# Optimization experiments

Measured on AMD Instinct MI355X. Metric: run time of the kernel, lower is better.

The kernel has to match this reference:

```python
import jax, jax.numpy as jnp
import numpy as np

B, L, E = 2, 2048, 1024
NH, DH = 16, 64          # num_heads, attn_hidden_size
HID = 4096               # FFN hidden_size
EPS = 1e-5


def _layernorm(x, g, b):
    mu = jnp.mean(x, axis=-1, keepdims=True)
    var = jnp.var(x, axis=-1, keepdims=True)
    return (x - mu) * jax.lax.rsqrt(var + EPS) * g + b


def setup_inputs() -> dict:
    key = jax.random.key(0)
    ks = jax.random.split(key, 12)
    s = 0.02
    return {
        "x":    jax.random.normal(ks[0], (B, L, E), dtype=jnp.float32),
        "Wa":   jax.random.normal(ks[1], (E, NH * 3 * DH), dtype=jnp.float32) * s,
        "Wout": jax.random.normal(ks[2], (NH * DH, E), dtype=jnp.float32) * s,
        "bout": jnp.zeros((E,), dtype=jnp.float32),
        "W1":   jax.random.normal(ks[3], (E, HID), dtype=jnp.float32) * s,
        "b1":   jnp.zeros((HID,), dtype=jnp.float32),
        "W2":   jax.random.normal(ks[4], (HID, E), dtype=jnp.float32) * s,
        "b2":   jnp.zeros((E,), dtype=jnp.float32),
        "g1":   jnp.ones((E,), dtype=jnp.float32),
        "be1":  jnp.zeros((E,), dtype=jnp.float32),
        "g2":   jnp.ones((E,), dtype=jnp.float32),
        "be2":  jnp.zeros((E,), dtype=jnp.float32),
    }


def _attention(o, Wa, Wout, bout):
    b, l, e = o.shape
    tmp = o @ Wa                                   # (b, l, nh*3*dh)
    tmp = tmp.reshape(b, l, NH, 3 * DH).transpose(0, 2, 1, 3)  # (b, nh, l, 3dh)
    q, k, v = jnp.split(tmp, 3, axis=-1)           # each (b, nh, l, dh)
    scores = jnp.einsum('bhqd,bhkd->bhqk', q, k) / np.sqrt(DH)
    causal = jnp.tril(jnp.ones((l, l), dtype=bool))
    scores = jnp.where(causal, scores, -jnp.inf)
    A = jax.nn.softmax(scores, axis=-1)
    out = jnp.einsum('bhqk,bhkd->bhqd', A, v)      # (b, nh, l, dh)
    out = out.transpose(0, 2, 1, 3).reshape(b, l, NH * DH)
    return out @ Wout + bout


def reference(x, Wa, Wout, bout, W1, b1, W2, b2, g1, be1, g2, be2):
    o = _layernorm(x, g1, be1)
    o = _attention(o, Wa, Wout, bout)
    o = _layernorm(x + o, g2, be2)
    o = o @ W1 + b1          # activation is Identity
    o = x + (o @ W2 + b2)
    return o
```

## Files before the change

### kernel.cpp

```cpp
#include <hip/hip_runtime.h>
#include <hip/hip_bf16.h>

#define BB 2
#define LL 2048
#define EE 1024
#define NHH 16
#define DHH 64
#define HIDD 4096
#define MTOK (BB*LL)
#define NQKV (NHH*3*DHH)

typedef __attribute__((ext_vector_type(8))) short bf16x8;
typedef __attribute__((ext_vector_type(4))) float f32x4;

#define MFMA16(a,b,c) __builtin_amdgcn_mfma_f32_16x16x32_bf16(a,b,c,0,0,0)

static __device__ __forceinline__ void gload_lds16(const void* g, void* lds) {
  __builtin_amdgcn_global_load_lds(
      (const __attribute__((address_space(1))) unsigned int*)g,
      (__attribute__((address_space(3))) unsigned int*)lds, 16, 0, 0);
}

__global__ __launch_bounds__(256)
void convT_kernel(const float* __restrict__ W, __hip_bfloat16* __restrict__ WT,
                  int K, int N) {
  __shared__ float tile[32][33];
  const int tx = threadIdx.x & 31, ty = threadIdx.x >> 5;
  const int n0 = blockIdx.x * 32, k0 = blockIdx.y * 32;
#pragma unroll
  for (int i = 0; i < 4; ++i)
    tile[ty + i*8][tx] = W[(size_t)(k0 + ty + i*8) * N + n0 + tx];
  __syncthreads();
#pragma unroll
  for (int i = 0; i < 4; ++i)
    WT[(size_t)(n0 + ty + i*8) * K + k0 + tx] = __float2bfloat16(tile[tx][ty + i*8]);
}

__global__ __launch_bounds__(256)
void vtrans_kernel(const __hip_bfloat16* __restrict__ qkv,
                   __hip_bfloat16* __restrict__ VT) {
  __shared__ ushort tile[32][34];
  const int tx = threadIdx.x & 31, ty = threadIdx.x >> 5;
  const int tok0 = blockIdx.x * 32;
  const int dh0  = blockIdx.y * 32;
  const int bh   = blockIdx.z;
  const int b = bh >> 4, h = bh & 15;
  const ushort* src = (const ushort*)qkv;
#pragma unroll
  for (int i = 0; i < 4; ++i)
    tile[ty + i*8][tx] =
      src[(size_t)(b*LL + tok0 + ty + i*8) * NQKV + h*192 + 128 + dh0 + tx];
  __syncthreads();
  ushort* dst = (ushort*)VT;
#pragma unroll
  for (int i = 0; i < 4; ++i)
    dst[(size_t)(bh*DHH + dh0 + ty + i*8) * LL + tok0 + tx] = tile[tx][ty + i*8];
}

__global__ __launch_bounds__(256)
void ln_kernel(const float* __restrict__ in, const float* __restrict__ g,
               const float* __restrict__ be, __hip_bfloat16* __restrict__ out) {
  const int row = blockIdx.x;
  const int t = threadIdx.x;
  const float4 v = ((const float4*)(in + (size_t)row * EE))[t];
  float s = v.x + v.y + v.z + v.w;
  float q = v.x*v.x + v.y*v.y + v.z*v.z + v.w*v.w;
#pragma unroll
  for (int off = 32; off >= 1; off >>= 1) {
    s += __shfl_xor(s, off);
    q += __shfl_xor(q, off);
  }
  __shared__ float ps[4], pq[4];
  if ((t & 63) == 0) { ps[t >> 6] = s; pq[t >> 6] = q; }
  __syncthreads();
  s = ps[0] + ps[1] + ps[2] + ps[3];
  q = pq[0] + pq[1] + pq[2] + pq[3];
  const float mean = s * (1.0f / EE);
  const float rstd = rsqrtf(q * (1.0f / EE) - mean * mean + 1e-5f);
  const float4 gg = ((const float4*)g)[t];
  const float4 bb = ((const float4*)be)[t];
  union { ushort4 u; __hip_bfloat16 h[4]; } o;
  o.h[0] = __float2bfloat16((v.x - mean) * rstd * gg.x + bb.x);
  o.h[1] = __float2bfloat16((v.y - mean) * rstd * gg.y + bb.y);
  o.h[2] = __float2bfloat16((v.z - mean) * rstd * gg.z + bb.z);
  o.h[3] = __float2bfloat16((v.w - mean) * rstd * gg.w + bb.w);
  ((ushort4*)(out + (size_t)row * EE))[t] = o.u;
}

template<int OUT_BF16, int HAS_BIAS, int HAS_RES>
__global__ __launch_bounds__(256)
void gemm_kernel(const __hip_bfloat16* __restrict__ A,
                 const __hip_bfloat16* __restrict__ BT,
                 void* __restrict__ Cv,
                 const float* __restrict__ bias,
                 const float* __restrict__ res,
                 int M, int N, int K) {
  __shared__ alignas(16) __hip_bfloat16 sA[128 * 32];
  __shared__ alignas(16) __hip_bfloat16 sB[128 * 32];
  const int t = threadIdx.x;
  const int wv = t >> 6;
  const int l = t & 63;
  const int lr = l & 15;
  const int lk = (l >> 4) * 8;
  const int m0 = blockIdx.y * 128;
  const int n0 = blockIdx.x * 128;
  const int wrow = (wv >> 1) * 64;
  const int wcol = (wv & 1) * 64;

  const int srow = t >> 2;
  const int scol = (t & 3) * 8;
  const __hip_bfloat16* gA = A + (size_t)(m0 + srow) * K + scol;
  const __hip_bfloat16* gB = BT + (size_t)(n0 + srow) * K + scol;
  char* ldsA = (char*)sA + wv * 1024;
  char* ldsB = (char*)sB + wv * 1024;

  f32x4 acc[4][4] = {};

  for (int k0 = 0; k0 < K; k0 += 32) {
    gload_lds16(gA + k0, ldsA);
    gload_lds16(gA + (size_t)64 * K + k0, ldsA + 4096);
    gload_lds16(gB + k0, ldsB);
    gload_lds16(gB + (size_t)64 * K + k0, ldsB + 4096);
    __syncthreads();
    bf16x8 af[4], bfv[4];
#pragma unroll
    for (int mi = 0; mi < 4; ++mi)
      af[mi] = *(const bf16x8*)(sA + (wrow + mi * 16 + lr) * 32 + lk);
#pragma unroll
    for (int ni = 0; ni < 4; ++ni)
      bfv[ni] = *(const bf16x8*)(sB + (wcol + ni * 16 + lr) * 32 + lk);
#pragma unroll
    for (int mi = 0; mi < 4; ++mi)
#pragma unroll
      for (int ni = 0; ni < 4; ++ni)
        acc[mi][ni] = MFMA16(af[mi], bfv[ni], acc[mi][ni]);
    __syncthreads();
  }

  const int rbase = (l >> 4) * 4;
#pragma unroll
  for (int mi = 0; mi < 4; ++mi) {
#pragma unroll
    for (int ni = 0; ni < 4; ++ni) {
#pragma unroll
      for (int r = 0; r < 4; ++r) {
        const int row = m0 + wrow + mi * 16 + rbase + r;
        const int col = n0 + wcol + ni * 16 + lr;
        float v = acc[mi][ni][r];
        if constexpr (HAS_BIAS) v += bias[col];
        if constexpr (HAS_RES)  v += res[(size_t)row * N + col];
        if constexpr (OUT_BF16)
          ((__hip_bfloat16*)Cv)[(size_t)row * N + col] = __float2bfloat16(v);
        else
          ((float*)Cv)[(size_t)row * N + col] = v;
      }
    }
  }
}

__global__ __launch_bounds__(256)
void attn_kernel(const __hip_bfloat16* __restrict__ qkv,
                 const __hip_bfloat16* __restrict__ VT,
                 __hip_bfloat16* __restrict__ out) {
  __shared__ alignas(16) __hip_bfloat16 sP[4][32 * 72];
  const int t = threadIdx.x;
  const int wv = t >> 6, l = t & 63;
  const int lr = l & 15, lg = l >> 4, lk = lg * 8;
  const int hh = blockIdx.y, b = blockIdx.z;
  int qx = blockIdx.x;
  if (b == 1) qx = 15 - qx;
  const int qw = qx * 128 + wv * 32;
  const size_t rowbase = (size_t)b * LL;
  const int hoff = hh * (3 * DHH);
  const __hip_bfloat16* vt = VT + (size_t)((b * NHH + hh) * DHH) * LL;

  bf16x8 qa[2][2];
#pragma unroll
  for (int rg = 0; rg < 2; ++rg)
#pragma unroll
    for (int h = 0; h < 2; ++h)
      qa[rg][h] = *(const bf16x8*)(qkv + (rowbase + qw + rg*16 + lr) * NQKV
                                   + hoff + h*32 + lk);

  f32x4 o[2][4] = {};
  float mrun[2][4], lrun[2][4];
#pragma unroll
  for (int rg = 0; rg < 2; ++rg)
#pragma unroll
    for (int r = 0; r < 4; ++r) { mrun[rg][r] = -INFINITY; lrun[rg][r] = 0.f; }

  __hip_bfloat16* sp = sP[wv];
  const int nt = (qw + 95) >> 6;

  for (int kt = 0; kt < nt; ++kt) {
    const int t0 = kt * 64;
    bf16x8 vb[4][2];
#pragma unroll
    for (int ni = 0; ni < 4; ++ni)
#pragma unroll
      for (int ks = 0; ks < 2; ++ks)
        vb[ni][ks] = *(const bf16x8*)(vt + (size_t)(ni*16 + lr) * LL + t0 + ks*32 + lk);

    f32x4 s[2][4];
#pragma unroll
    for (int tg = 0; tg < 4; ++tg) {
      const __hip_bfloat16* kp = qkv + (rowbase + t0 + tg*16 + lr) * NQKV + hoff + DHH;
      bf16x8 kb0 = *(const bf16x8*)(kp + lk);
      bf16x8 kb1 = *(const bf16x8*)(kp + 32 + lk);
#pragma unroll
      for (int rg = 0; rg < 2; ++rg) {
        f32x4 z = {0.f, 0.f, 0.f, 0.f};
        z = MFMA16(qa[rg][0], kb0, z);
        z = MFMA16(qa[rg][1], kb1, z);
        s[rg][tg] = z;
      }
    }

    const bool edge = (kt == nt - 1);
#pragma unroll
    for (int rg = 0; rg < 2; ++rg)
#pragma unroll
      for (int tg = 0; tg < 4; ++tg)
#pragma unroll
        for (int r = 0; r < 4; ++r) {
          float v = s[rg][tg][r] * 0.125f;
          if (edge) {
            const int tok = t0 + tg*16 + lr;
            const int qr  = qw + rg*16 + lg*4 + r;
            if (tok > qr) v = -INFINITY;
          }
          s[rg][tg][r] = v;
        }

#pragma unroll
    for (int rg = 0; rg < 2; ++rg)
#pragma unroll
      for (int r = 0; r < 4; ++r) {
        float m = fmaxf(fmaxf(s[rg][0][r], s[rg][1][r]),
                        fmaxf(s[rg][2][r], s[rg][3][r]));
#pragma unroll
        for (int off = 8; off >= 1; off >>= 1)
          m = fmaxf(m, __shfl_xor(m, off));
        const float mnew = fmaxf(mrun[rg][r], m);
        const float corr = __expf(mrun[rg][r] - mnew);
        const float p0 = __expf(s[rg][0][r] - mnew);
        const float p1 = __expf(s[rg][1][r] - mnew);
        const float p2 = __expf(s[rg][2][r] - mnew);
        const float p3 = __expf(s[rg][3][r] - mnew);
        float rs = (p0 + p1) + (p2 + p3);
#pragma unroll
        for (int off = 8; off >= 1; off >>= 1)
          rs += __shfl_xor(rs, off);
        lrun[rg][r] = lrun[rg][r] * corr + rs;
        mrun[rg][r] = mnew;
        const int q = rg*16 + lg*4 + r;
        sp[q*72 +      lr] = __float2bfloat16(p0);
        sp[q*72 + 16 + lr] = __float2bfloat16(p1);
        sp[q*72 + 32 + lr] = __float2bfloat16(p2);
        sp[q*72 + 48 + lr] = __float2bfloat16(p3);
#pragma unroll
        for (int ni = 0; ni < 4; ++ni) o[rg][ni][r] *= corr;
      }

#pragma unroll
    for (int rg = 0; rg < 2; ++rg) {
      bf16x8 pf0 = *(const bf16x8*)(sp + (rg*16 + lr)*72 + lk);
      bf16x8 pf1 = *(const bf16x8*)(sp + (rg*16 + lr)*72 + 32 + lk);
#pragma unroll
      for (int ni = 0; ni < 4; ++ni) {
        o[rg][ni] = MFMA16(pf0, vb[ni][0], o[rg][ni]);
        o[rg][ni] = MFMA16(pf1, vb[ni][1], o[rg][ni]);
      }
    }
  }

#pragma unroll
  for (int rg = 0; rg < 2; ++rg)
#pragma unroll
    for (int r = 0; r < 4; ++r) {
      const float inv = 1.0f / lrun[rg][r];
      const int qr = qw + rg*16 + lg*4 + r;
      __hip_bfloat16* op = out + (rowbase + qr) * (NHH * DHH) + hh * DHH;
#pragma unroll
      for (int ni = 0; ni < 4; ++ni)
        op[ni*16 + lr] = __float2bfloat16(o[rg][ni][r] * inv);
    }
}

extern "C" void kernel_launch(void* const* d_in, const int* in_sizes, int n_in,
                              void* d_out, int out_size, void* d_ws, size_t ws_size,
                              hipStream_t stream) {
  (void)in_sizes; (void)n_in; (void)out_size; (void)ws_size;
  const float* x    = (const float*)d_in[0];
  const float* Wa   = (const float*)d_in[1];
  const float* Wout = (const float*)d_in[2];
  const float* bout = (const float*)d_in[3];
  const float* W1   = (const float*)d_in[4];
  const float* b1   = (const float*)d_in[5];
  const float* W2   = (const float*)d_in[6];
  const float* b2   = (const float*)d_in[7];
  const float* g1   = (const float*)d_in[8];
  const float* be1  = (const float*)d_in[9];
  const float* g2   = (const float*)d_in[10];
  const float* be2  = (const float*)d_in[11];

  char* ws = (char*)d_ws;
  __hip_bfloat16* WaT   = (__hip_bfloat16*)(ws + 0);
  __hip_bfloat16* WoutT = (__hip_bfloat16*)(ws + 6291456);
  __hip_bfloat16* W1T   = (__hip_bfloat16*)(ws + 8388608);
  __hip_bfloat16* W2T   = (__hip_bfloat16*)(ws + 16777216);
  __hip_bfloat16* o1    = (__hip_bfloat16*)(ws + 25165824);
  __hip_bfloat16* qkv   = (__hip_bfloat16*)(ws + 33554432);
  __hip_bfloat16* hbuf  = (__hip_bfloat16*)(ws + 25165824);
  __hip_bfloat16* attnb = (__hip_bfloat16*)(ws + 58720256);
  __hip_bfloat16* ln2b  = (__hip_bfloat16*)(ws + 58720256);
  float*          ybuf  = (float*)(ws + 67108864);
  __hip_bfloat16* VT    = (__hip_bfloat16*)(ws + 67108864);

  convT_kernel<<<dim3(NQKV/32, EE/32), 256, 0, stream>>>(Wa, WaT, EE, NQKV);
  convT_kernel<<<dim3(EE/32, EE/32), 256, 0, stream>>>(Wout, WoutT, EE, EE);
  convT_kernel<<<dim3(HIDD/32, EE/32), 256, 0, stream>>>(W1, W1T, EE, HIDD);
  convT_kernel<<<dim3(EE/32, HIDD/32), 256, 0, stream>>>(W2, W2T, HIDD, EE);
  ln_kernel<<<MTOK, 256, 0, stream>>>(x, g1, be1, o1);
  gemm_kernel<1,0,0><<<dim3(NQKV/128, MTOK/128), 256, 0, stream>>>(
      o1, WaT, qkv, nullptr, nullptr, MTOK, NQKV, EE);
  vtrans_kernel<<<dim3(LL/32, DHH/32, BB*NHH), 256, 0, stream>>>(qkv, VT);
  attn_kernel<<<dim3(LL/128, NHH, BB), 256, 0, stream>>>(qkv, VT, attnb);
  gemm_kernel<0,1,1><<<dim3(EE/128, MTOK/128), 256, 0, stream>>>(
      attnb, WoutT, ybuf, bout, x, MTOK, EE, EE);
  ln_kernel<<<MTOK, 256, 0, stream>>>(ybuf, g2, be2, ln2b);
  gemm_kernel<1,1,0><<<dim3(HIDD/128, MTOK/128), 256, 0, stream>>>(
      ln2b, W1T, hbuf, b1, nullptr, MTOK, HIDD, EE);
  gemm_kernel<0,1,1><<<dim3(EE/128, MTOK/128), 256, 0, stream>>>(
      hbuf, W2T, (float*)d_out, b2, x, MTOK, EE, HIDD);
}
```

Baseline: 437.7 us.

## Double-buffer GEMM LDS tiles, swizzle workgroups, split-K the FFN2 GEMM

Rewrites the GEMM as a body with two LDS buffers so the next K-slice's global-to-LDS loads are issued while the current slice is computed. It also adds a workgroup index remap meant to improve L2 reuse. The FFN2 GEMM becomes a split-K launch with 128x64 tiles writing two fp32 partial buffers, followed by a reduction kernel that adds bias and residual; this targets the small-grid occupancy problem of the K=4096 GEMM at the cost of extra partial-buffer traffic. Workspace buffers are reassigned so the partials fit.

Result: faster. 402.4 us (-8.0%).

```diff
diff --git a/kernel.cpp b/kernel.cpp
--- a/kernel.cpp
+++ b/kernel.cpp
@@ -87,53 +87,65 @@
   ((ushort4*)(out + (size_t)row * EE))[t] = o.u;
 }
 
-template<int OUT_BF16, int HAS_BIAS, int HAS_RES>
-__global__ __launch_bounds__(256)
-void gemm_kernel(const __hip_bfloat16* __restrict__ A,
-                 const __hip_bfloat16* __restrict__ BT,
-                 void* __restrict__ Cv,
-                 const float* __restrict__ bias,
-                 const float* __restrict__ res,
-                 int M, int N, int K) {
-  __shared__ alignas(16) __hip_bfloat16 sA[128 * 32];
-  __shared__ alignas(16) __hip_bfloat16 sB[128 * 32];
+template<int BN, int OUT_BF16, int HAS_BIAS, int HAS_RES>
+__device__ __forceinline__ void gemm_body(
+    const __hip_bfloat16* __restrict__ A, const __hip_bfloat16* __restrict__ BT,
+    void* __restrict__ Cv, const float* __restrict__ bias,
+    const float* __restrict__ res, int M, int N, int K, int lda, int ldb) {
+  constexpr int NF = BN / 32;
+  __shared__ alignas(16) __hip_bfloat16 sA[2][128 * 32];
+  __shared__ alignas(16) __hip_bfloat16 sB[2][BN * 32];
   const int t = threadIdx.x;
-  const int wv = t >> 6;
-  const int l = t & 63;
-  const int lr = l & 15;
-  const int lk = (l >> 4) * 8;
-  const int m0 = blockIdx.y * 128;
-  const int n0 = blockIdx.x * 128;
+  const int wv = t >> 6, l = t & 63;
+  const int lr = l & 15, lk = (l >> 4) * 8;
+
+  const int nwg = gridDim.x * gridDim.y;
+  int wg = blockIdx.y * gridDim.x + blockIdx.x;
+  wg = (wg & 7) * (nwg >> 3) + (wg >> 3);
+  const int bx = wg % gridDim.x, by = wg / gridDim.x;
+  const int m0 = by * 128, n0 = bx * BN;
+
   const int wrow = (wv >> 1) * 64;
-  const int wcol = (wv & 1) * 64;
-
-  const int srow = t >> 2;
-  const int scol = (t & 3) * 8;
-  const __hip_bfloat16* gA = A + (size_t)(m0 + srow) * K + scol;
-  const __hip_bfloat16* gB = BT + (size_t)(n0 + srow) * K + scol;
-  char* ldsA = (char*)sA + wv * 1024;
-  char* ldsB = (char*)sB + wv * 1024;
-
-  f32x4 acc[4][4] = {};
-
-  for (int k0 = 0; k0 < K; k0 += 32) {
-    gload_lds16(gA + k0, ldsA);
-    gload_lds16(gA + (size_t)64 * K + k0, ldsA + 4096);
-    gload_lds16(gB + k0, ldsB);
-    gload_lds16(gB + (size_t)64 * K + k0, ldsB + 4096);
+  const int wcol = (wv & 1) * (BN / 2);
+  const int srow = t >> 2, scol = (t & 3) * 8;
+  const __hip_bfloat16* gA = A + (size_t)(m0 + srow) * lda + scol;
+  const __hip_bfloat16* gB = BT + (size_t)(n0 + srow) * ldb + scol;
+
+  auto stage = [&](int buf, int k0) {
+    char* dA = (char*)(&sA[buf][0]) + wv * 1024;
+    gload_lds16(gA + k0, dA);
+    gload_lds16(gA + (size_t)64 * lda + k0, dA + 4096);
+    char* dB = (char*)(&sB[buf][0]) + wv * 1024;
+    gload_lds16(gB + k0, dB);
+    if constexpr (BN == 128)
+      gload_lds16(gB + (size_t)64 * ldb + k0, dB + 4096);
+  };
+
+  f32x4 acc[4][NF] = {};
+
+  auto compute = [&](int buf) {
+    bf16x8 af[4], bfv[NF];
+#pragma unroll
+    for (int mi = 0; mi < 4; ++mi)
+      af[mi] = *(const bf16x8*)(&sA[buf][(wrow + mi * 16 + lr) * 32 + lk]);
+#pragma unroll
+    for (int ni = 0; ni < NF; ++ni)
+      bfv[ni] = *(const bf16x8*)(&sB[buf][(wcol + ni * 16 + lr) * 32 + lk]);
+#pragma unroll
+    for (int mi = 0; mi < 4; ++mi)
+#pragma unroll
+      for (int ni = 0; ni < NF; ++ni)
+        acc[mi][ni] = MFMA16(af[mi], bfv[ni], acc[mi][ni]);
+  };
+
+  stage(0, 0);
+  __syncthreads();
+  for (int k0 = 0; k0 < K; k0 += 64) {
+    stage(1, k0 + 32);
+    compute(0);
     __syncthreads();
-    bf16x8 af[4], bfv[4];
-#pragma unroll
-    for (int mi = 0; mi < 4; ++mi)
-      af[mi] = *(const bf16x8*)(sA + (wrow + mi * 16 + lr) * 32 + lk);
-#pragma unroll
-    for (int ni = 0; ni < 4; ++ni)
-      bfv[ni] = *(const bf16x8*)(sB + (wcol + ni * 16 + lr) * 32 + lk);
-#pragma unroll
-    for (int mi = 0; mi < 4; ++mi)
-#pragma unroll
-      for (int ni = 0; ni < 4; ++ni)
-        acc[mi][ni] = MFMA16(af[mi], bfv[ni], acc[mi][ni]);
+    if (k0 + 64 < K) stage(0, k0 + 64);
+    compute(1);
     __syncthreads();
   }
 
@@ -141,7 +153,7 @@
 #pragma unroll
   for (int mi = 0; mi < 4; ++mi) {
 #pragma unroll
-    for (int ni = 0; ni < 4; ++ni) {
+    for (int ni = 0; ni < NF; ++ni) {
 #pragma unroll
       for (int r = 0; r < 4; ++r) {
         const int row = m0 + wrow + mi * 16 + rbase + r;
@@ -155,6 +167,46 @@
           ((float*)Cv)[(size_t)row * N + col] = v;
       }
     }
+  }
+}
+
+__global__ __launch_bounds__(256)
+void gemm_qkv(const __hip_bfloat16* A, const __hip_bfloat16* BT, __hip_bfloat16* C) {
+  gemm_body<128,1,0,0>(A, BT, C, nullptr, nullptr, MTOK, NQKV, EE, EE, EE);
+}
+__global__ __launch_bounds__(256)
+void gemm_wout(const __hip_bfloat16* A, const __hip_bfloat16* BT, float* C,
+               const float* bias, const float* res) {
+  gemm_body<128,0,1,1>(A, BT, C, bias, res, MTOK, EE, EE, EE, EE);
+}
+__global__ __launch_bounds__(256)
+void gemm_ffn1(const __hip_bfloat16* A, const __hip_bfloat16* BT, __hip_bfloat16* C,
+               const float* bias) {
+  gemm_body<128,1,1,0>(A, BT, C, bias, nullptr, MTOK, HIDD, EE, EE, EE);
+}
+__global__ __launch_bounds__(256)
+void gemm_ffn2p(const __hip_bfloat16* A, const __hip_bfloat16* BT,
+                float* P0, float* P1) {
+  const int ks = blockIdx.z;
+  float* P = ks ? P1 : P0;
+  gemm_body<64,0,0,0>(A + ks * 2048, BT + ks * 2048, P, nullptr, nullptr,
+                      MTOK, EE, 2048, HIDD, HIDD);
+}
+
+__global__ __launch_bounds__(256)
+void ffn2_reduce(const float4* __restrict__ P0, const float4* __restrict__ P1,
+                 const float4* __restrict__ x, const float* __restrict__ b2,
+                 float4* __restrict__ out) {
+  const int n4 = MTOK * EE / 4;
+  for (int i = blockIdx.x * 256 + threadIdx.x; i < n4; i += 2048 * 256) {
+    const float4 b = ((const float4*)b2)[i & 255];
+    const float4 p = P0[i], q = P1[i], xx = x[i];
+    float4 o;
+    o.x = xx.x + b.x + p.x + q.x;
+    o.y = xx.y + b.y + p.y + q.y;
+    o.z = xx.z + b.z + p.z + q.z;
+    o.w = xx.w + b.w + p.w + q.w;
+    out[i] = o;
   }
 }
 
@@ -311,26 +363,26 @@
   __hip_bfloat16* W2T   = (__hip_bfloat16*)(ws + 16777216);
   __hip_bfloat16* o1    = (__hip_bfloat16*)(ws + 25165824);
   __hip_bfloat16* qkv   = (__hip_bfloat16*)(ws + 33554432);
-  __hip_bfloat16* hbuf  = (__hip_bfloat16*)(ws + 25165824);
-  __hip_bfloat16* attnb = (__hip_bfloat16*)(ws + 58720256);
-  __hip_bfloat16* ln2b  = (__hip_bfloat16*)(ws + 58720256);
-  float*          ybuf  = (float*)(ws + 67108864);
-  __hip_bfloat16* VT    = (__hip_bfloat16*)(ws + 67108864);
+  __hip_bfloat16* VT    = (__hip_bfloat16*)(ws + 58720256);
+  __hip_bfloat16* attnb = (__hip_bfloat16*)(ws + 67108864);
+  float*          ybuf  = (float*)(ws + 33554432);
+  __hip_bfloat16* ln2b  = (__hip_bfloat16*)(ws + 25165824);
+  __hip_bfloat16* hbuf  = (__hip_bfloat16*)(ws + 50331648);
+  float*          P0    = (float*)(ws + 0);
+  float*          P1    = (float*)(ws + 33554432);
 
   convT_kernel<<<dim3(NQKV/32, EE/32), 256, 0, stream>>>(Wa, WaT, EE, NQKV);
   convT_kernel<<<dim3(EE/32, EE/32), 256, 0, stream>>>(Wout, WoutT, EE, EE);
   convT_kernel<<<dim3(HIDD/32, EE/32), 256, 0, stream>>>(W1, W1T, EE, HIDD);
   convT_kernel<<<dim3(EE/32, HIDD/32), 256, 0, stream>>>(W2, W2T, HIDD, EE);
   ln_kernel<<<MTOK, 256, 0, stream>>>(x, g1, be1, o1);
-  gemm_kernel<1,0,0><<<dim3(NQKV/128, MTOK/128), 256, 0, stream>>>(
-      o1, WaT, qkv, nullptr, nullptr, MTOK, NQKV, EE);
+  gemm_qkv<<<dim3(NQKV/128, MTOK/128), 256, 0, stream>>>(o1, WaT, qkv);
   vtrans_kernel<<<dim3(LL/32, DHH/32, BB*NHH), 256, 0, stream>>>(qkv, VT);
   attn_kernel<<<dim3(LL/128, NHH, BB), 256, 0, stream>>>(qkv, VT, attnb);
-  gemm_kernel<0,1,1><<<dim3(EE/128, MTOK/128), 256, 0, stream>>>(
-      attnb, WoutT, ybuf, bout, x, MTOK, EE, EE);
+  gemm_wout<<<dim3(EE/128, MTOK/128), 256, 0, stream>>>(attnb, WoutT, ybuf, bout, x);
   ln_kernel<<<MTOK, 256, 0, stream>>>(ybuf, g2, be2, ln2b);
-  gemm_kernel<1,1,0><<<dim3(HIDD/128, MTOK/128), 256, 0, stream>>>(
-      ln2b, W1T, hbuf, b1, nullptr, MTOK, HIDD, EE);
-  gemm_kernel<0,1,1><<<dim3(EE/128, MTOK/128), 256, 0, stream>>>(
-      hbuf, W2T, (float*)d_out, b2, x, MTOK, EE, HIDD);
-}
+  gemm_ffn1<<<dim3(HIDD/128, MTOK/128), 256, 0, stream>>>(ln2b, W1T, hbuf, b1);
+  gemm_ffn2p<<<dim3(EE/64, MTOK/128, 2), 256, 0, stream>>>(hbuf, W2T, P0, P1);
+  ffn2_reduce<<<2048, 256, 0, stream>>>((const float4*)P0, (const float4*)P1,
+                                        (const float4*)x, b2, (float4*)d_out);
+}
```
